# Kernel optimization log

Hardware: AMD Instinct MI355X
Metric: run time of the kernel (lower is better)

## Reference

```python
import jax, jax.numpy as jnp
import numpy as np

IN_FEATURES = 4096
OUT_FEATURES = 14336
GROUP_SIZE = 128  # in_features grouped: 4096 / 128 = 32 groups
N_GROUPS = IN_FEATURES // GROUP_SIZE


def setup_inputs() -> dict:
    key = jax.random.key(0)
    k_x, k_q, k_s, k_zb, k_b = jax.random.split(key, 5)
    x = jax.random.normal(k_x, (8, 32, IN_FEATURES), dtype=jnp.float32)
    # uint8-style affine-quantized weights packed as (in_features, out_features)
    quant_kernel = jax.random.randint(k_q, (IN_FEATURES, OUT_FEATURES), 0, 256, dtype=jnp.int32)
    # per-group scales / zero-point biases: (n_groups, out_features)
    quant_scales = (jax.random.uniform(k_s, (N_GROUPS, OUT_FEATURES), dtype=jnp.float32) + 0.5) * 0.01
    quant_biases = jax.random.normal(k_zb, (N_GROUPS, OUT_FEATURES), dtype=jnp.float32) * 0.01
    bias = jax.random.normal(k_b, (OUT_FEATURES,), dtype=jnp.float32) * 0.02
    return {"x": x, "quant_kernel": quant_kernel, "quant_scales": quant_scales,
            "quant_biases": quant_biases, "bias": bias}


def reference(x, quant_kernel, quant_scales, quant_biases, bias):
    # Affine group-wise dequant: w[f, o] = q[f, o] * scale[f//G, o] + zp_bias[f//G, o]
    q = quant_kernel.astype(jnp.float32).reshape(N_GROUPS, GROUP_SIZE, OUT_FEATURES)
    w = q * quant_scales[:, None, :] + quant_biases[:, None, :]
    w = w.reshape(IN_FEATURES, OUT_FEATURES)
    # y = x @ W + b  (x: [B, S, K], W: [K, N])
    y = jnp.einsum("bsk,kn->bsn", x, w) + bias
    return y
```

## Files before the change

### kernel.cpp

```cpp
#include <hip/hip_runtime.h>
#include <hip/hip_bf16.h>

#define K_DIM 4096
#define N_DIM 14336
#define M_DIM 256
#define BM 128
#define BN 64
#define BK 64
#define NPH 64
#define WRS 72

typedef __attribute__((ext_vector_type(4))) float f32x4;
typedef __attribute__((ext_vector_type(8))) short short8;

__device__ __forceinline__ unsigned short f2bf(float f) {
    union { float f; unsigned u; } v; v.f = f;
    unsigned r = v.u + 0x7fffu + ((v.u >> 16) & 1u);
    return (unsigned short)(r >> 16);
}

__device__ __forceinline__ void glds16(const void* g, void* l) {
    __builtin_amdgcn_global_load_lds(
        (const __attribute__((address_space(1))) void*)g,
        (__attribute__((address_space(3))) void*)l, 16, 0, 0);
}

#define KBAR(N) do { \
    asm volatile("s_waitcnt lgkmcnt(0)" ::: "memory");     \
    asm volatile("s_waitcnt vmcnt(" #N ")" ::: "memory");  \
    __builtin_amdgcn_s_barrier();                           \
} while (0)

__global__ void convert_x_kernel(const float* __restrict__ x,
                                 unsigned short* __restrict__ xf) {
    int t = blockIdx.x * blockDim.x + threadIdx.x;
    int chunk = t >> 6;
    int lane  = t & 63;
    int ktile = chunk >> 4;
    int mtile = chunk & 15;
    int m = mtile * 16 + (lane & 15);
    int k = ktile * 32 + ((lane >> 4) << 3);
    const float* xp = x + (size_t)m * K_DIM + k;
    float4 lo = *(const float4*)xp;
    float4 hi = *(const float4*)(xp + 4);
    union { unsigned short s[8]; int4 v; } o;
    o.s[0] = f2bf(lo.x); o.s[1] = f2bf(lo.y); o.s[2] = f2bf(lo.z); o.s[3] = f2bf(lo.w);
    o.s[4] = f2bf(hi.x); o.s[5] = f2bf(hi.y); o.s[6] = f2bf(hi.z); o.s[7] = f2bf(hi.w);
    *(int4*)(xf + ((size_t)t << 3)) = o.v;
}

__global__ __launch_bounds__(512, 4)
void plq_gemm_v9(const unsigned short* __restrict__ xf,
                 const int* __restrict__ q,
                 const float* __restrict__ qs,
                 const float* __restrict__ qb,
                 const float* __restrict__ bias,
                 float* __restrict__ out)
{
    __shared__ int            qt[3][BK * BN];
    __shared__ unsigned short wt[2][BN * WRS];
    __shared__ unsigned       szb[32 * BN];

    const int tid  = threadIdx.x;
    const int lane = tid & 63;
    const int wv   = tid >> 6;
    const int wm   = wv >> 1;
    const int wn   = wv & 1;

    const int gid = (blockIdx.x & 7) * 56 + (blockIdx.x >> 3);
    const int mh  = gid & 1;
    const int n0  = (gid >> 1) * BN;

    const size_t qvoff = (size_t)(8 * wv + (lane >> 4)) * N_DIM + n0 + ((lane & 15) << 2);
    const int n_d  = tid & 63;
    const int k0_d = (tid >> 6) << 3;

    f32x4 acc[2][2] = {};
    short8 afX[2][2], afY[2][2];

    auto issueQ = [&](int t, int slot) {
        const int* s0 = q + (size_t)t * BK * N_DIM + qvoff;
        char* d = (char*)&qt[slot][0] + (wv << 11);
        glds16(s0, d);
        glds16(s0 + (size_t)4 * N_DIM, d + 1024);
    };
    auto loadAf = [&](int t, short8 (&af)[2][2]) {
        #pragma unroll
        for (int ks = 0; ks < 2; ++ks)
            #pragma unroll
            for (int mf = 0; mf < 2; ++mf) {
                const int chunk = (2 * t + ks) * 16 + (mh * 8 + wm * 2 + mf);
                af[ks][mf] = *(const short8*)(xf + ((size_t)chunk << 9) + (lane << 3));
            }
    };
    auto dequant = [&](int t, int slot) {
        const int* qp = &qt[slot][0];
        int v[8];
        #pragma unroll
        for (int j = 0; j < 8; ++j) v[j] = qp[(k0_d + j) * BN + n_d];
        const unsigned szp = szb[((t >> 1) << 6) + n_d];
        union { unsigned u; float f; } su, zu;
        su.u = szp << 16;
        zu.u = szp & 0xffff0000u;
        union { unsigned u[4]; int4 vv; } pk;
        #pragma unroll
        for (int j = 0; j < 4; ++j) {
            float f0 = (float)v[2*j]   * su.f + zu.f;
            float f1 = (float)v[2*j+1] * su.f + zu.f;
            pk.u[j] = (unsigned)f2bf(f0) | ((unsigned)f2bf(f1) << 16);
        }
        *(int4*)&wt[t & 1][n_d * WRS + k0_d] = pk.vv;
    };
    auto mfma = [&](const short8 (&af)[2][2], const unsigned short* wbuf) {
        #pragma unroll
        for (int ks = 0; ks < 2; ++ks) {
            const int kb = ks * 32 + ((lane >> 4) << 3);
            short8 b0 = *(const short8*)&wbuf[(wn * 32 +      (lane & 15)) * WRS + kb];
            short8 b1 = *(const short8*)&wbuf[(wn * 32 + 16 + (lane & 15)) * WRS + kb];
            acc[0][0] = __builtin_amdgcn_mfma_f32_16x16x32_bf16(af[ks][0], b0, acc[0][0], 0, 0, 0);
            acc[0][1] = __builtin_amdgcn_mfma_f32_16x16x32_bf16(af[ks][0], b1, acc[0][1], 0, 0, 0);
            acc[1][0] = __builtin_amdgcn_mfma_f32_16x16x32_bf16(af[ks][1], b0, acc[1][0], 0, 0, 0);
            acc[1][1] = __builtin_amdgcn_mfma_f32_16x16x32_bf16(af[ks][1], b1, acc[1][1], 0, 0, 0);
        }
    };

    #pragma unroll
    for (int j = 0; j < 4; ++j) {
        const int idx = tid + j * 512;
        const int g = idx >> 6, n = idx & 63;
        float s = qs[(size_t)g * N_DIM + n0 + n];
        float z = qb[(size_t)g * N_DIM + n0 + n];
        szb[idx] = (unsigned)f2bf(s) | ((unsigned)f2bf(z) << 16);
    }
    issueQ(0, 0);
    issueQ(1, 1);
    loadAf(0, afX);
    KBAR(6);
    dequant(0, 0);
    issueQ(2, 2);
    KBAR(6);

    #pragma unroll 1
    for (int ii = 0; ii < 32; ++ii) {
        const int i = ii << 1;

        if (i + 3 < NPH) issueQ(i + 3, (i + 3) % 3);
        loadAf(i + 1, afY);
        dequant(i + 1, (i + 1) % 3);
        mfma(afX, &wt[i & 1][0]);
        KBAR(6);

        if (i + 4 < NPH) issueQ(i + 4, (i + 4) % 3);
        if (i + 2 < NPH) loadAf(i + 2, afX);
        if (i + 2 < NPH) dequant(i + 2, (i + 2) % 3);
        mfma(afY, &wt[(i + 1) & 1][0]);
        KBAR(6);
    }

    #pragma unroll
    for (int nf = 0; nf < 2; ++nf) {
        const int n = n0 + wn * 32 + nf * 16 + (lane & 15);
        const float bv = bias[n];
        #pragma unroll
        for (int mf = 0; mf < 2; ++mf) {
            const int m0 = mh * BM + wm * 32 + mf * 16 + ((lane >> 4) << 2);
            #pragma unroll
            for (int r = 0; r < 4; ++r)
                out[(size_t)(m0 + r) * N_DIM + n] = acc[mf][nf][r] + bv;
        }
    }
}

#define FBN 64
#define FBK 128
#define FNITER 32
#define FRS 136
__global__ __launch_bounds__(512, 2)
void plq_gemm_fb(const float* __restrict__ x,
                 const int* __restrict__ q,
                 const float* __restrict__ qs,
                 const float* __restrict__ qb,
                 const float* __restrict__ bias,
                 float* __restrict__ out)
{
    __shared__ unsigned short wlds[2][FBN * FRS];
    const int tid  = threadIdx.x;
    const int lane = tid & 63;
    const int wv   = tid >> 6;
    const int wm   = wv >> 1;
    const int wn   = wv & 1;
    const int n0   = blockIdx.x * FBN;
    const int nl = (tid & 31) * 2;
    const int kl = (tid >> 5) * 8;

    f32x4 acc[4][2] = {};
    int2   qr[8];
    float2 sv, zv;

    auto loadq = [&](int i) {
        const int* qp = q + (size_t)(i * FBK + kl) * N_DIM + (n0 + nl);
        #pragma unroll
        for (int j = 0; j < 8; ++j) qr[j] = *(const int2*)(qp + (size_t)j * N_DIM);
        sv = *(const float2*)(qs + (size_t)i * N_DIM + (n0 + nl));
        zv = *(const float2*)(qb + (size_t)i * N_DIM + (n0 + nl));
    };
    auto deqw = [&](int b) {
        union { unsigned u[4]; int4 v; } p0, p1;
        #pragma unroll
        for (int j = 0; j < 4; ++j) {
            float a0 = (float)qr[2*j].x   * sv.x + zv.x;
            float a1 = (float)qr[2*j+1].x * sv.x + zv.x;
            float c0 = (float)qr[2*j].y   * sv.y + zv.y;
            float c1 = (float)qr[2*j+1].y * sv.y + zv.y;
            p0.u[j] = (unsigned)f2bf(a0) | ((unsigned)f2bf(a1) << 16);
            p1.u[j] = (unsigned)f2bf(c0) | ((unsigned)f2bf(c1) << 16);
        }
        *(int4*)&wlds[b][(nl + 0) * FRS + kl] = p0.v;
        *(int4*)&wlds[b][(nl + 1) * FRS + kl] = p1.v;
    };
    auto compute = [&](int i, int cur) {
        short8 afr[4][4];
        #pragma unroll
        for (int ks = 0; ks < 4; ++ks)
            #pragma unroll
            for (int mf = 0; mf < 4; ++mf) {
                int m = wm * 64 + mf * 16 + (lane & 15);
                int k = i * FBK + ks * 32 + ((lane >> 4) << 3);
                const float* xp = x + (size_t)m * K_DIM + k;
                float4 lo = *(const float4*)xp;
                float4 hi = *(const float4*)(xp + 4);
                union { unsigned short s[8]; short8 v; } u;
                u.s[0] = f2bf(lo.x); u.s[1] = f2bf(lo.y); u.s[2] = f2bf(lo.z); u.s[3] = f2bf(lo.w);
                u.s[4] = f2bf(hi.x); u.s[5] = f2bf(hi.y); u.s[6] = f2bf(hi.z); u.s[7] = f2bf(hi.w);
                afr[ks][mf] = u.v;
            }
        #pragma unroll
        for (int ks = 0; ks < 4; ++ks) {
            const int kb = ks * 32 + ((lane >> 4) << 3);
            short8 b0 = *(const short8*)&wlds[cur][(wn * 32 +      (lane & 15)) * FRS + kb];
            short8 b1 = *(const short8*)&wlds[cur][(wn * 32 + 16 + (lane & 15)) * FRS + kb];
            #pragma unroll
            for (int mf = 0; mf < 4; ++mf) {
                acc[mf][0] = __builtin_amdgcn_mfma_f32_16x16x32_bf16(afr[ks][mf], b0, acc[mf][0], 0, 0, 0);
                acc[mf][1] = __builtin_amdgcn_mfma_f32_16x16x32_bf16(afr[ks][mf], b1, acc[mf][1], 0, 0, 0);
            }
        }
    };

    loadq(0); deqw(0); __syncthreads();
    for (int i = 0; i < FNITER; ++i) {
        const int cur = i & 1;
        if (i + 1 < FNITER) loadq(i + 1);
        compute(i, cur);
        if (i + 1 < FNITER) deqw(cur ^ 1);
        __syncthreads();
    }
    #pragma unroll
    for (int nf = 0; nf < 2; ++nf) {
        const int n = n0 + wn * 32 + nf * 16 + (lane & 15);
        const float bb = bias[n];
        #pragma unroll
        for (int mf = 0; mf < 4; ++mf) {
            const int m0 = wm * 64 + mf * 16 + ((lane >> 4) << 2);
            #pragma unroll
            for (int r = 0; r < 4; ++r)
                out[(size_t)(m0 + r) * N_DIM + n] = acc[mf][nf][r] + bb;
        }
    }
}

extern "C" void kernel_launch(void* const* d_in, const int* in_sizes, int n_in,
                              void* d_out, int out_size, void* d_ws, size_t ws_size,
                              hipStream_t stream) {
    const float* x    = (const float*)d_in[0];
    const int*   qk   = (const int*)d_in[1];
    const float* qs   = (const float*)d_in[2];
    const float* qb   = (const float*)d_in[3];
    const float* bias = (const float*)d_in[4];
    float* out = (float*)d_out;

    const size_t xf_bytes = (size_t)M_DIM * K_DIM * sizeof(unsigned short);
    if (ws_size >= xf_bytes) {
        unsigned short* xf = (unsigned short*)d_ws;
        convert_x_kernel<<<512, 256, 0, stream>>>(x, xf);
        const int grid = (M_DIM / BM) * (N_DIM / BN);
        plq_gemm_v9<<<grid, 512, 0, stream>>>(xf, qk, qs, qb, bias, out);
    } else {
        plq_gemm_fb<<<N_DIM / FBN, 512, 0, stream>>>(x, qk, qs, qb, bias, out);
    }
}
```

Baseline: 96.80 us.

## Factor group scale and zero-point out of GEMM via raw-int MFMA

Rewrites the dequant GEMM algebraically. It multiplies x by the raw integer weights, converted to bf16 by truncation through a byte permute, into a per-group accumulator that is scaled once per group. The zero-point term is added at the end as a small GEMM of per-group x sums against the zero-point biases. This removes the per-element scale/zero FMA and the bf16 re-store of dequantized weights to LDS. It also changes the pipeline to a 4-stage async load of both A and the q tiles with BK=32. The risk is that truncating ints 0-255 to bf16 loses precision, and that bf16-rounded group sums add error.

```diff
diff --git a/kernel.cpp b/kernel.cpp
--- a/kernel.cpp
+++ b/kernel.cpp
@@ -6,9 +6,9 @@
 #define M_DIM 256
 #define BM 128
 #define BN 64
-#define BK 64
-#define NPH 64
-#define WRS 72
+#define BK 32
+#define PH 128
+#define NG 32
 
 typedef __attribute__((ext_vector_type(4))) float f32x4;
 typedef __attribute__((ext_vector_type(8))) short short8;
@@ -49,121 +49,143 @@
     *(int4*)(xf + ((size_t)t << 3)) = o.v;
 }
 
+__global__ void xg_kernel(const float* __restrict__ x,
+                          unsigned short* __restrict__ xg) {
+    __shared__ float part[128];
+    const int m = blockIdx.x, t = threadIdx.x;
+    const float* xp = x + (size_t)m * K_DIM + t * 32;
+    float s = 0.f;
+    #pragma unroll
+    for (int j = 0; j < 32; j += 4) {
+        float4 v = *(const float4*)(xp + j);
+        s += v.x + v.y + v.z + v.w;
+    }
+    part[t] = s;
+    __syncthreads();
+    if (t < NG) {
+        float g = part[4*t] + part[4*t+1] + part[4*t+2] + part[4*t+3];
+        xg[(size_t)m * NG + t] = f2bf(g);
+    }
+}
+
 __global__ __launch_bounds__(512, 4)
-void plq_gemm_v9(const unsigned short* __restrict__ xf,
-                 const int* __restrict__ q,
-                 const float* __restrict__ qs,
-                 const float* __restrict__ qb,
-                 const float* __restrict__ bias,
-                 float* __restrict__ out)
+void plq_gemm_v10(const unsigned short* __restrict__ xf,
+                  const unsigned short* __restrict__ xg,
+                  const int* __restrict__ q,
+                  const float* __restrict__ qs,
+                  const float* __restrict__ qb,
+                  const float* __restrict__ bias,
+                  float* __restrict__ out)
 {
-    __shared__ int            qt[3][BK * BN];
-    __shared__ unsigned short wt[2][BN * WRS];
-    __shared__ unsigned       szb[32 * BN];
+    __shared__ int            qt[4][BK * BN];
+    __shared__ unsigned short at[4][BM * BK];
+    __shared__ float          sl[NG * BN];
 
     const int tid  = threadIdx.x;
     const int lane = tid & 63;
     const int wv   = tid >> 6;
     const int wm   = wv >> 1;
     const int wn   = wv & 1;
+    const int l4   = lane >> 4;
+    const int lc   = lane & 15;
 
     const int gid = (blockIdx.x & 7) * 56 + (blockIdx.x >> 3);
     const int mh  = gid & 1;
     const int n0  = (gid >> 1) * BN;
 
-    const size_t qvoff = (size_t)(8 * wv + (lane >> 4)) * N_DIM + n0 + ((lane & 15) << 2);
-    const int n_d  = tid & 63;
-    const int k0_d = (tid >> 6) << 3;
-
-    f32x4 acc[2][2] = {};
-    short8 afX[2][2], afY[2][2];
-
-    auto issueQ = [&](int t, int slot) {
-        const int* s0 = q + (size_t)t * BK * N_DIM + qvoff;
-        char* d = (char*)&qt[slot][0] + (wv << 11);
-        glds16(s0, d);
-        glds16(s0 + (size_t)4 * N_DIM, d + 1024);
-    };
-    auto loadAf = [&](int t, short8 (&af)[2][2]) {
-        #pragma unroll
-        for (int ks = 0; ks < 2; ++ks)
+    const f32x4 vzero = {0.f, 0.f, 0.f, 0.f};
+    f32x4 acc[2][2] = {}, gacc[2][2] = {};
+
+    auto issueT = [&](int t) {
+        const int* qsrc = q + (size_t)(t * BK + 4 * wv + l4) * N_DIM + n0 + lc * 4;
+        glds16(qsrc, (char*)&qt[t & 3][0] + (wv << 10));
+        const unsigned short* asrc = xf + ((size_t)(t * 16 + mh * 8 + wv) << 9) + (lane << 3);
+        glds16(asrc, (char*)&at[t & 3][0] + (wv << 10));
+    };
+
+    auto compute = [&](int slot) {
+        short8 a0 = *(const short8*)&at[slot][(wm * 2 + 0) * 512 + (lane << 3)];
+        short8 a1 = *(const short8*)&at[slot][(wm * 2 + 1) * 512 + (lane << 3)];
+        #pragma unroll
+        for (int nf = 0; nf < 2; ++nf) {
+            const int cb = wn * 32 + nf * 16 + lc;
+            unsigned u[8];
+            #pragma unroll
+            for (int j = 0; j < 8; ++j) {
+                float fv = (float)qt[slot][(l4 * 8 + j) * BN + cb];
+                union { float f; unsigned w; } cv; cv.f = fv;
+                u[j] = cv.w;
+            }
+            union { unsigned w[4]; short8 s; } b;
+            b.w[0] = __builtin_amdgcn_perm(u[1], u[0], 0x07060302u);
+            b.w[1] = __builtin_amdgcn_perm(u[3], u[2], 0x07060302u);
+            b.w[2] = __builtin_amdgcn_perm(u[5], u[4], 0x07060302u);
+            b.w[3] = __builtin_amdgcn_perm(u[7], u[6], 0x07060302u);
+            gacc[0][nf] = __builtin_amdgcn_mfma_f32_16x16x32_bf16(a0, b.s, gacc[0][nf], 0, 0, 0);
+            gacc[1][nf] = __builtin_amdgcn_mfma_f32_16x16x32_bf16(a1, b.s, gacc[1][nf], 0, 0, 0);
+        }
+    };
+
+    auto applyS = [&](int g) {
+        #pragma unroll
+        for (int nf = 0; nf < 2; ++nf) {
+            float s = sl[g * BN + wn * 32 + nf * 16 + lc];
             #pragma unroll
             for (int mf = 0; mf < 2; ++mf) {
-                const int chunk = (2 * t + ks) * 16 + (mh * 8 + wm * 2 + mf);
-                af[ks][mf] = *(const short8*)(xf + ((size_t)chunk << 9) + (lane << 3));
-            }
-    };
-    auto dequant = [&](int t, int slot) {
-        const int* qp = &qt[slot][0];
-        int v[8];
-        #pragma unroll
-        for (int j = 0; j < 8; ++j) v[j] = qp[(k0_d + j) * BN + n_d];
-        const unsigned szp = szb[((t >> 1) << 6) + n_d];
-        union { unsigned u; float f; } su, zu;
-        su.u = szp << 16;
-        zu.u = szp & 0xffff0000u;
-        union { unsigned u[4]; int4 vv; } pk;
-        #pragma unroll
-        for (int j = 0; j < 4; ++j) {
-            float f0 = (float)v[2*j]   * su.f + zu.f;
-            float f1 = (float)v[2*j+1] * su.f + zu.f;
-            pk.u[j] = (unsigned)f2bf(f0) | ((unsigned)f2bf(f1) << 16);
-        }
-        *(int4*)&wt[t & 1][n_d * WRS + k0_d] = pk.vv;
-    };
-    auto mfma = [&](const short8 (&af)[2][2], const unsigned short* wbuf) {
-        #pragma unroll
-        for (int ks = 0; ks < 2; ++ks) {
-            const int kb = ks * 32 + ((lane >> 4) << 3);
-            short8 b0 = *(const short8*)&wbuf[(wn * 32 +      (lane & 15)) * WRS + kb];
-            short8 b1 = *(const short8*)&wbuf[(wn * 32 + 16 + (lane & 15)) * WRS + kb];
-            acc[0][0] = __builtin_amdgcn_mfma_f32_16x16x32_bf16(af[ks][0], b0, acc[0][0], 0, 0, 0);
-            acc[0][1] = __builtin_amdgcn_mfma_f32_16x16x32_bf16(af[ks][0], b1, acc[0][1], 0, 0, 0);
-            acc[1][0] = __builtin_amdgcn_mfma_f32_16x16x32_bf16(af[ks][1], b0, acc[1][0], 0, 0, 0);
-            acc[1][1] = __builtin_amdgcn_mfma_f32_16x16x32_bf16(af[ks][1], b1, acc[1][1], 0, 0, 0);
+                acc[mf][nf] += gacc[mf][nf] * s;
+                gacc[mf][nf] = vzero;
+            }
         }
     };
 
     #pragma unroll
     for (int j = 0; j < 4; ++j) {
-        const int idx = tid + j * 512;
-        const int g = idx >> 6, n = idx & 63;
-        float s = qs[(size_t)g * N_DIM + n0 + n];
-        float z = qb[(size_t)g * N_DIM + n0 + n];
-        szb[idx] = (unsigned)f2bf(s) | ((unsigned)f2bf(z) << 16);
-    }
-    issueQ(0, 0);
-    issueQ(1, 1);
-    loadAf(0, afX);
-    KBAR(6);
-    dequant(0, 0);
-    issueQ(2, 2);
-    KBAR(6);
+        int idx = tid + j * 512;
+        sl[idx] = qs[(size_t)(idx >> 6) * N_DIM + n0 + (idx & 63)];
+    }
+    issueT(0); issueT(1); issueT(2);
+    KBAR(4);
 
     #pragma unroll 1
-    for (int ii = 0; ii < 32; ++ii) {
-        const int i = ii << 1;
-
-        if (i + 3 < NPH) issueQ(i + 3, (i + 3) % 3);
-        loadAf(i + 1, afY);
-        dequant(i + 1, (i + 1) % 3);
-        mfma(afX, &wt[i & 1][0]);
-        KBAR(6);
-
-        if (i + 4 < NPH) issueQ(i + 4, (i + 4) % 3);
-        if (i + 2 < NPH) loadAf(i + 2, afX);
-        if (i + 2 < NPH) dequant(i + 2, (i + 2) % 3);
-        mfma(afY, &wt[(i + 1) & 1][0]);
-        KBAR(6);
+    for (int g = 0; g < 31; ++g) {
+        const int p = g * 4;
+        issueT(p + 3); compute(0); KBAR(4);
+        issueT(p + 4); compute(1); KBAR(4);
+        issueT(p + 5); compute(2); KBAR(4);
+        issueT(p + 6); compute(3); KBAR(4);
+        applyS(g);
+    }
+    issueT(127); compute(0); KBAR(4);
+    compute(1); KBAR(2);
+    compute(2); KBAR(0);
+    compute(3);
+    applyS(31);
+
+    {
+        short8 xa0 = *(const short8*)(xg + (size_t)(mh * 128 + wm * 32 + 0 * 16 + lc) * NG + l4 * 8);
+        short8 xa1 = *(const short8*)(xg + (size_t)(mh * 128 + wm * 32 + 1 * 16 + lc) * NG + l4 * 8);
+        #pragma unroll
+        for (int nf = 0; nf < 2; ++nf) {
+            const int n = n0 + wn * 32 + nf * 16 + lc;
+            union { unsigned w[4]; short8 s; } b;
+            #pragma unroll
+            for (int j = 0; j < 4; ++j) {
+                float z0 = qb[(size_t)(l4 * 8 + 2 * j)     * N_DIM + n];
+                float z1 = qb[(size_t)(l4 * 8 + 2 * j + 1) * N_DIM + n];
+                b.w[j] = (unsigned)f2bf(z0) | ((unsigned)f2bf(z1) << 16);
+            }
+            acc[0][nf] = __builtin_amdgcn_mfma_f32_16x16x32_bf16(xa0, b.s, acc[0][nf], 0, 0, 0);
+            acc[1][nf] = __builtin_amdgcn_mfma_f32_16x16x32_bf16(xa1, b.s, acc[1][nf], 0, 0, 0);
+        }
     }
 
     #pragma unroll
     for (int nf = 0; nf < 2; ++nf) {
-        const int n = n0 + wn * 32 + nf * 16 + (lane & 15);
+        const int n = n0 + wn * 32 + nf * 16 + lc;
         const float bv = bias[n];
         #pragma unroll
         for (int mf = 0; mf < 2; ++mf) {
-            const int m0 = mh * BM + wm * 32 + mf * 16 + ((lane >> 4) << 2);
+            const int m0 = mh * 128 + wm * 32 + mf * 16 + l4 * 4;
             #pragma unroll
             for (int r = 0; r < 4; ++r)
                 out[(size_t)(m0 + r) * N_DIM + n] = acc[mf][nf][r] + bv;
@@ -280,11 +302,14 @@
     float* out = (float*)d_out;
 
     const size_t xf_bytes = (size_t)M_DIM * K_DIM * sizeof(unsigned short);
-    if (ws_size >= xf_bytes) {
+    const size_t xg_bytes = (size_t)M_DIM * NG * sizeof(unsigned short);
+    if (ws_size >= xf_bytes + xg_bytes) {
         unsigned short* xf = (unsigned short*)d_ws;
+        unsigned short* xg = (unsigned short*)((char*)d_ws + xf_bytes);
         convert_x_kernel<<<512, 256, 0, stream>>>(x, xf);
+        xg_kernel<<<M_DIM, 128, 0, stream>>>(x, xg);
         const int grid = (M_DIM / BM) * (N_DIM / BN);
-        plq_gemm_v9<<<grid, 512, 0, stream>>>(xf, qk, qs, qb, bias, out);
+        plq_gemm_v10<<<grid, 512, 0, stream>>>(xf, xg, qk, qs, qb, bias, out);
     } else {
         plq_gemm_fb<<<N_DIM / FBN, 512, 0, stream>>>(x, qk, qs, qb, bias, out);
     }
```

After: 118.3 us. +22.2%, slower.

## Replace async LDS triple-buffer with register-prefetched dequant and BK=128 tiles

Applied to the files above, without the earlier changes.

The main GEMM kernel stops using global_load_lds into a triple-buffered int LDS stage with hand-placed waitcnt barriers. Quantized weights are now prefetched into registers as int2 pairs one tile ahead, dequantized directly with fp32 scales and zero points, packed to bf16 with a perm (truncation instead of round-to-nearest), and written to a double-buffered LDS tile of BK=128. This cuts LDS traffic and the scale/zero staging setup, and halves the number of barriers. In exchange it raises register pressure (occupancy hint drops from 4 to 2 blocks) and depends on the compiler to overlap the global loads.

```diff
diff --git a/kernel.cpp b/kernel.cpp
--- a/kernel.cpp
+++ b/kernel.cpp
@@ -6,9 +6,9 @@
 #define M_DIM 256
 #define BM 128
 #define BN 64
-#define BK 64
-#define NPH 64
-#define WRS 72
+#define BK 128
+#define NITER 32
+#define FRS 136
 
 typedef __attribute__((ext_vector_type(4))) float f32x4;
 typedef __attribute__((ext_vector_type(8))) short short8;
@@ -18,18 +18,6 @@
     unsigned r = v.u + 0x7fffu + ((v.u >> 16) & 1u);
     return (unsigned short)(r >> 16);
 }
-
-__device__ __forceinline__ void glds16(const void* g, void* l) {
-    __builtin_amdgcn_global_load_lds(
-        (const __attribute__((address_space(1))) void*)g,
-        (__attribute__((address_space(3))) void*)l, 16, 0, 0);
-}
-
-#define KBAR(N) do { \
-    asm volatile("s_waitcnt lgkmcnt(0)" ::: "memory");     \
-    asm volatile("s_waitcnt vmcnt(" #N ")" ::: "memory");  \
-    __builtin_amdgcn_s_barrier();                           \
-} while (0)
 
 __global__ void convert_x_kernel(const float* __restrict__ x,
                                  unsigned short* __restrict__ xf) {
@@ -49,74 +37,73 @@
     *(int4*)(xf + ((size_t)t << 3)) = o.v;
 }
 
-__global__ __launch_bounds__(512, 4)
-void plq_gemm_v9(const unsigned short* __restrict__ xf,
-                 const int* __restrict__ q,
-                 const float* __restrict__ qs,
-                 const float* __restrict__ qb,
-                 const float* __restrict__ bias,
-                 float* __restrict__ out)
+__global__ __launch_bounds__(512, 2)
+void plq_gemm_v11(const unsigned short* __restrict__ xf,
+                  const int* __restrict__ q,
+                  const float* __restrict__ qs,
+                  const float* __restrict__ qb,
+                  const float* __restrict__ bias,
+                  float* __restrict__ out)
 {
-    __shared__ int            qt[3][BK * BN];
-    __shared__ unsigned short wt[2][BN * WRS];
-    __shared__ unsigned       szb[32 * BN];
+    __shared__ unsigned short wlds[2][BN * FRS];
 
     const int tid  = threadIdx.x;
     const int lane = tid & 63;
     const int wv   = tid >> 6;
     const int wm   = wv >> 1;
     const int wn   = wv & 1;
+    const int l4   = lane >> 4;
+    const int lc   = lane & 15;
 
     const int gid = (blockIdx.x & 7) * 56 + (blockIdx.x >> 3);
     const int mh  = gid & 1;
     const int n0  = (gid >> 1) * BN;
 
-    const size_t qvoff = (size_t)(8 * wv + (lane >> 4)) * N_DIM + n0 + ((lane & 15) << 2);
-    const int n_d  = tid & 63;
-    const int k0_d = (tid >> 6) << 3;
+    const int nl = (tid & 31) * 2;
+    const int kl = (tid >> 5) * 8;
 
     f32x4 acc[2][2] = {};
-    short8 afX[2][2], afY[2][2];
-
-    auto issueQ = [&](int t, int slot) {
-        const int* s0 = q + (size_t)t * BK * N_DIM + qvoff;
-        char* d = (char*)&qt[slot][0] + (wv << 11);
-        glds16(s0, d);
-        glds16(s0 + (size_t)4 * N_DIM, d + 1024);
-    };
-    auto loadAf = [&](int t, short8 (&af)[2][2]) {
-        #pragma unroll
-        for (int ks = 0; ks < 2; ++ks)
+    short8 afX[4][2], afY[4][2];
+    int2   qr[8];
+    float2 sv, zv;
+
+    auto loadQ = [&](int i) {
+        const int* qp = q + (size_t)(i * BK + kl) * N_DIM + (n0 + nl);
+        #pragma unroll
+        for (int j = 0; j < 8; ++j) qr[j] = *(const int2*)(qp + (size_t)j * N_DIM);
+        sv = *(const float2*)(qs + (size_t)i * N_DIM + (n0 + nl));
+        zv = *(const float2*)(qb + (size_t)i * N_DIM + (n0 + nl));
+    };
+    auto loadAf = [&](int i, short8 (&af)[4][2]) {
+        #pragma unroll
+        for (int ks = 0; ks < 4; ++ks)
             #pragma unroll
             for (int mf = 0; mf < 2; ++mf) {
-                const int chunk = (2 * t + ks) * 16 + (mh * 8 + wm * 2 + mf);
+                const int chunk = (i * 4 + ks) * 16 + (mh * 8 + wm * 2 + mf);
                 af[ks][mf] = *(const short8*)(xf + ((size_t)chunk << 9) + (lane << 3));
             }
     };
-    auto dequant = [&](int t, int slot) {
-        const int* qp = &qt[slot][0];
-        int v[8];
-        #pragma unroll
-        for (int j = 0; j < 8; ++j) v[j] = qp[(k0_d + j) * BN + n_d];
-        const unsigned szp = szb[((t >> 1) << 6) + n_d];
-        union { unsigned u; float f; } su, zu;
-        su.u = szp << 16;
-        zu.u = szp & 0xffff0000u;
-        union { unsigned u[4]; int4 vv; } pk;
+    auto deq = [&](int b) {
+        union { unsigned u[4]; int4 v; } p0, p1;
         #pragma unroll
         for (int j = 0; j < 4; ++j) {
-            float f0 = (float)v[2*j]   * su.f + zu.f;
-            float f1 = (float)v[2*j+1] * su.f + zu.f;
-            pk.u[j] = (unsigned)f2bf(f0) | ((unsigned)f2bf(f1) << 16);
-        }
-        *(int4*)&wt[t & 1][n_d * WRS + k0_d] = pk.vv;
-    };
-    auto mfma = [&](const short8 (&af)[2][2], const unsigned short* wbuf) {
-        #pragma unroll
-        for (int ks = 0; ks < 2; ++ks) {
-            const int kb = ks * 32 + ((lane >> 4) << 3);
-            short8 b0 = *(const short8*)&wbuf[(wn * 32 +      (lane & 15)) * WRS + kb];
-            short8 b1 = *(const short8*)&wbuf[(wn * 32 + 16 + (lane & 15)) * WRS + kb];
+            union { float f; unsigned w; } a0, a1, c0, c1;
+            a0.f = (float)qr[2*j].x   * sv.x + zv.x;
+            a1.f = (float)qr[2*j+1].x * sv.x + zv.x;
+            c0.f = (float)qr[2*j].y   * sv.y + zv.y;
+            c1.f = (float)qr[2*j+1].y * sv.y + zv.y;
+            p0.u[j] = __builtin_amdgcn_perm(a1.w, a0.w, 0x07060302u);
+            p1.u[j] = __builtin_amdgcn_perm(c1.w, c0.w, 0x07060302u);
+        }
+        *(int4*)&wlds[b][(nl + 0) * FRS + kl] = p0.v;
+        *(int4*)&wlds[b][(nl + 1) * FRS + kl] = p1.v;
+    };
+    auto compute = [&](const short8 (&af)[4][2], int cur) {
+        #pragma unroll
+        for (int ks = 0; ks < 4; ++ks) {
+            const int kb = ks * 32 + l4 * 8;
+            short8 b0 = *(const short8*)&wlds[cur][(wn * 32 +      lc) * FRS + kb];
+            short8 b1 = *(const short8*)&wlds[cur][(wn * 32 + 16 + lc) * FRS + kb];
             acc[0][0] = __builtin_amdgcn_mfma_f32_16x16x32_bf16(af[ks][0], b0, acc[0][0], 0, 0, 0);
             acc[0][1] = __builtin_amdgcn_mfma_f32_16x16x32_bf16(af[ks][0], b1, acc[0][1], 0, 0, 0);
             acc[1][0] = __builtin_amdgcn_mfma_f32_16x16x32_bf16(af[ks][1], b0, acc[1][0], 0, 0, 0);
@@ -124,46 +111,33 @@
         }
     };
 
-    #pragma unroll
-    for (int j = 0; j < 4; ++j) {
-        const int idx = tid + j * 512;
-        const int g = idx >> 6, n = idx & 63;
-        float s = qs[(size_t)g * N_DIM + n0 + n];
-        float z = qb[(size_t)g * N_DIM + n0 + n];
-        szb[idx] = (unsigned)f2bf(s) | ((unsigned)f2bf(z) << 16);
-    }
-    issueQ(0, 0);
-    issueQ(1, 1);
+    loadQ(0);
     loadAf(0, afX);
-    KBAR(6);
-    dequant(0, 0);
-    issueQ(2, 2);
-    KBAR(6);
+    deq(0);
+    __syncthreads();
 
     #pragma unroll 1
-    for (int ii = 0; ii < 32; ++ii) {
+    for (int ii = 0; ii < 16; ++ii) {
         const int i = ii << 1;
 
-        if (i + 3 < NPH) issueQ(i + 3, (i + 3) % 3);
-        loadAf(i + 1, afY);
-        dequant(i + 1, (i + 1) % 3);
-        mfma(afX, &wt[i & 1][0]);
-        KBAR(6);
-
-        if (i + 4 < NPH) issueQ(i + 4, (i + 4) % 3);
-        if (i + 2 < NPH) loadAf(i + 2, afX);
-        if (i + 2 < NPH) dequant(i + 2, (i + 2) % 3);
-        mfma(afY, &wt[(i + 1) & 1][0]);
-        KBAR(6);
+        if (i + 1 < NITER) { loadQ(i + 1); loadAf(i + 1, afY); }
+        compute(afX, 0);
+        if (i + 1 < NITER) deq(1);
+        __syncthreads();
+
+        if (i + 2 < NITER) { loadQ(i + 2); loadAf(i + 2, afX); }
+        compute(afY, 1);
+        if (i + 2 < NITER) deq(0);
+        __syncthreads();
     }
 
     #pragma unroll
     for (int nf = 0; nf < 2; ++nf) {
-        const int n = n0 + wn * 32 + nf * 16 + (lane & 15);
+        const int n = n0 + wn * 32 + nf * 16 + lc;
         const float bv = bias[n];
         #pragma unroll
         for (int mf = 0; mf < 2; ++mf) {
-            const int m0 = mh * BM + wm * 32 + mf * 16 + ((lane >> 4) << 2);
+            const int m0 = mh * BM + wm * 32 + mf * 16 + l4 * 4;
             #pragma unroll
             for (int r = 0; r < 4; ++r)
                 out[(size_t)(m0 + r) * N_DIM + n] = acc[mf][nf][r] + bv;
@@ -174,7 +148,6 @@
 #define FBN 64
 #define FBK 128
 #define FNITER 32
-#define FRS 136
 __global__ __launch_bounds__(512, 2)
 void plq_gemm_fb(const float* __restrict__ x,
                  const int* __restrict__ q,
@@ -284,7 +257,7 @@
         unsigned short* xf = (unsigned short*)d_ws;
         convert_x_kernel<<<512, 256, 0, stream>>>(x, xf);
         const int grid = (M_DIM / BM) * (N_DIM / BN);
-        plq_gemm_v9<<<grid, 512, 0, stream>>>(xf, qk, qs, qb, bias, out);
+        plq_gemm_v11<<<grid, 512, 0, stream>>>(xf, qk, qs, qb, bias, out);
     } else {
         plq_gemm_fb<<<N_DIM / FBN, 512, 0, stream>>>(x, qk, qs, qb, bias, out);
     }
```

Result: slower. 124.4 us (+28.5%).
